# Kernel optimization log

Measured on AMD Instinct MI355X. Metric: run time of the kernel, lower is better.

The kernel has to match this reference:

```python
import jax, jax.numpy as jnp
import numpy as np

B, P, D = 8, 1024, 1024
H, N = 16, 64  # num_heads, head_dim


def setup_inputs() -> dict:
    key = jax.random.key(0)
    k1, k2, k3 = jax.random.split(key, 3)
    inputs = jax.random.normal(k1, (B, P, D), dtype=jnp.float32)
    # Keras 'random_normal' initializer: stddev 0.05
    w_qkv = jax.random.normal(k2, (H, 3, D, N), dtype=jnp.float32) * 0.05
    w_o = jax.random.normal(k3, (N * H, D), dtype=jnp.float32) * 0.05
    return {"inputs": inputs, "w_qkv": w_qkv, "w_o": w_o}


def reference(inputs, w_qkv, w_o):
    # Per-head QKV projection: [b,p,d] x [h,3,d,n] -> [b,h,3,p,n]
    proj = jnp.einsum('bpv,havn->bhapn', inputs, w_qkv)
    q = proj[:, :, 0]  # [b,h,p,n]
    k = proj[:, :, 1]
    v = proj[:, :, 2]
    head_dim = q.shape[-1]
    scale = 1.0 / jnp.sqrt(jnp.asarray(head_dim, dtype=jnp.float32))
    scores = jnp.einsum('bhqn,bhkn->bhqk', q, k) * scale  # [b,h,p,p]
    attn = jax.nn.softmax(scores, axis=-1)
    out = jnp.einsum('bhqk,bhkn->bhqn', attn, v)  # [b,h,p,n]
    # concat heads along feature dim: [b,p,h*n]
    b, h, p, n = out.shape
    concat = out.transpose(0, 2, 1, 3).reshape(b, p, h * n)
    return jnp.einsum('bpi,ij->bpj', concat, w_o)  # [b,p,d_model]
```

## Files before the change

kernel.cpp:

```cpp
#include <hip/hip_runtime.h>
#include <stdint.h>

typedef _Float16 f16;
typedef __attribute__((ext_vector_type(2))) _Float16 f16x2;
typedef __attribute__((ext_vector_type(4))) _Float16 f16x4;
typedef __attribute__((ext_vector_type(8))) _Float16 f16x8;
typedef __attribute__((ext_vector_type(2))) __fp16 h16x2;
typedef __attribute__((ext_vector_type(4))) float f32x4;
typedef __attribute__((ext_vector_type(16))) float f32x16;
typedef __attribute__((ext_vector_type(4))) uint32_t u32x4;

__device__ __forceinline__ void gload_lds16(const void* g, void* l) {
  __builtin_amdgcn_global_load_lds(
      (__attribute__((address_space(1))) void*)const_cast<void*>(g),
      (__attribute__((address_space(3))) void*)l, 16, 0, 0);
}


__global__ void convert_x(const float* __restrict__ in, f16* __restrict__ out) {
  int i = blockIdx.x * 256 + threadIdx.x;
  float4 v = ((const float4*)in)[i];
  f16x4 hv;
  hv[0] = (f16)v.x; hv[1] = (f16)v.y; hv[2] = (f16)v.z; hv[3] = (f16)v.w;
  ((f16x4*)out)[i] = hv;
}

__global__ void transpose_wqkv(const float* __restrict__ in, f16* __restrict__ out) {
  __shared__ float tile[64][65];
  int s = blockIdx.x >> 4;
  int vt = blockIdx.x & 15;
  int hh = s / 3, a = s - hh * 3;
  int tx = threadIdx.x & 63, ty = threadIdx.x >> 6;
#pragma unroll
  for (int i = 0; i < 16; i++) {
    int r = i * 4 + ty;
    tile[r][tx] = in[((size_t)(s * 1024 + vt * 64 + r)) * 64 + tx];
  }
  __syncthreads();
#pragma unroll
  for (int i = 0; i < 16; i++) {
    int n = i * 4 + ty;
    out[((size_t)(a * 1024 + hh * 64 + n)) * 1024 + vt * 64 + tx] = (f16)tile[tx][n];
  }
}

__global__ void transpose_wo(const float* __restrict__ in, f16* __restrict__ out) {
  __shared__ float tile[64][65];
  int rt = blockIdx.x >> 4, ct = blockIdx.x & 15;
  int tx = threadIdx.x & 63, ty = threadIdx.x >> 6;
#pragma unroll
  for (int i = 0; i < 16; i++) {
    int r = i * 4 + ty;
    tile[r][tx] = in[((size_t)(rt * 64 + r)) * 1024 + ct * 64 + tx];
  }
  __syncthreads();
#pragma unroll
  for (int i = 0; i < 16; i++) {
    int j = i * 4 + ty;
    out[((size_t)(ct * 64 + j)) * 1024 + rt * 64 + tx] = (f16)tile[tx][j];
  }
}

template <int OUTMODE>
__global__ __launch_bounds__(256, 4) void gemm_kernel(
    const f16* __restrict__ A, const f16* __restrict__ BT, void* __restrict__ out,
    void* __restrict__ out2, int M, int N, int K) {
  __shared__ __align__(16) f16 As[128][64];
  __shared__ __align__(16) f16 Bs[128][64];
  const int t = threadIdx.x;
  const int lane = t & 63, wave = t >> 6;
  const int lr = lane & 15, lg = lane >> 4;
  const int wm = wave >> 1, wn = wave & 1;
  const int nTN = N >> 7;
  const int bm = blockIdx.x / nTN, bn = blockIdx.x % nTN;
  const f16* Ab = A + (size_t)bm * 128 * K;
  const f16* Bb = BT + (size_t)bn * 128 * K;

  const f32x4 zero4 = {0.f, 0.f, 0.f, 0.f};
  f32x4 acc[4][4];
#pragma unroll
  for (int m = 0; m < 4; m++)
#pragma unroll
    for (int n = 0; n < 4; n++) acc[m][n] = zero4;

  for (int k0 = 0; k0 < K; k0 += 64) {
    __syncthreads();
#pragma unroll
    for (int i = 0; i < 4; i++) {
      int q = wave * 4 + i;
      int u = q * 64 + lane;
      int r = u >> 3, j = u & 7;
      gload_lds16(Ab + (size_t)r * K + k0 + ((j ^ (r & 7)) << 3),
                  (char*)&As[0][0] + q * 1024);
      gload_lds16(Bb + (size_t)r * K + k0 + ((j ^ (r & 7)) << 3),
                  (char*)&Bs[0][0] + q * 1024);
    }
    __syncthreads();
#pragma unroll
    for (int half = 0; half < 2; half++) {
      f16x8 af[4], bf[4];
#pragma unroll
      for (int m = 0; m < 4; m++) {
        int r = wm * 64 + m * 16 + lr;
        af[m] = *(const f16x8*)&As[r][((half * 4 + lg) ^ (r & 7)) << 3];
      }
#pragma unroll
      for (int n = 0; n < 4; n++) {
        int r = wn * 64 + n * 16 + lr;
        bf[n] = *(const f16x8*)&Bs[r][((half * 4 + lg) ^ (r & 7)) << 3];
      }
#pragma unroll
      for (int m = 0; m < 4; m++)
#pragma unroll
        for (int n = 0; n < 4; n++)
          acc[m][n] = __builtin_amdgcn_mfma_f32_16x16x32_f16(af[m], bf[n], acc[m][n], 0, 0, 0);
    }
  }

  const int r0 = bm * 128 + wm * 64;
  const int c0 = bn * 128 + wn * 64;
  if (OUTMODE == 2 && bn >= 16) {
    f16* VT = (f16*)out2;
    const int bb = bm >> 3;
#pragma unroll
    for (int m = 0; m < 4; m++) {
      int pl = (r0 + m * 16 + lg * 4) & 1023;
      int pl2 = (pl & ~12) | ((pl & 4) << 1) | ((pl & 8) >> 1);
#pragma unroll
      for (int n = 0; n < 4; n++) {
        int vcol = c0 - 2048 + n * 16 + lr;
        f16x4 pv;
#pragma unroll
        for (int i = 0; i < 4; i++) pv[i] = (f16)acc[m][n][i];
        *(f16x4*)&VT[((size_t)(bb * 16 + (vcol >> 6)) * 64 + (vcol & 63)) * 1024 + pl2] = pv;
      }
    }
  } else {
#pragma unroll
    for (int m = 0; m < 4; m++)
#pragma unroll
      for (int n = 0; n < 4; n++)
#pragma unroll
        for (int i = 0; i < 4; i++) {
          int gr = r0 + m * 16 + lg * 4 + i;
          int gc = c0 + n * 16 + lr;
          if (OUTMODE == 1)
            ((float*)out)[(size_t)gr * N + gc] = acc[m][n][i];
          else
            ((f16*)out)[(size_t)gr * N + gc] = (f16)acc[m][n][i];
        }
  }
}

__global__ __launch_bounds__(256, 3) void attn_kernel(
    const f16* __restrict__ QKV, const f16* __restrict__ VT, f16* __restrict__ C) {
  __shared__ __align__(16) f16 smem[16384];

  const int t = threadIdx.x, lane = t & 63, wave = t >> 6;
  const int q = lane & 31, hi = lane >> 5, q7 = lane & 7;
  const int pt = blockIdx.x, bh = blockIdx.y;
  const int b = bh >> 4, h = bh & 15;
  const int p0 = pt * 128;

  const f16* Qg = QKV + ((size_t)(b * 1024 + p0)) * 3072 + h * 64;
  const f16* Kg = QKV + ((size_t)(b * 1024)) * 3072 + 1024 + h * 64;
  const f16* Vg = VT + (size_t)bh * 64 * 1024;

#pragma unroll
  for (int i = 0; i < 4; i++) {
    int qn = wave * 4 + i;
    int u = qn * 64 + lane;
    int r = u >> 3, j = u & 7;
    gload_lds16(Qg + (size_t)r * 3072 + ((j ^ (r & 7)) << 3), (char*)smem + qn * 1024);
  }
  __syncthreads();

  const f16 qscale = (f16)0.180336878f;
  f16x8 qB[4];
  {
    int rq = wave * 32 + q;
#pragma unroll
    for (int w = 0; w < 4; w++) {
      int cb = (2 * w + hi) ^ q7;
      f16x8 v = *(const f16x8*)&smem[(size_t)rq * 64 + (cb << 3)];
#pragma unroll
      for (int e = 0; e < 8; e++) v[e] *= qscale;
      qB[w] = v;
    }
  }
  __syncthreads();

  auto STAGE = [&](int kc, int cur) {
#pragma unroll
    for (int i = 0; i < 2; i++) {
      int qn = wave * 2 + i;
      int u = qn * 64 + lane;
      int r = u >> 3, j = u & 7;
      gload_lds16(Kg + (size_t)(kc * 64 + r) * 3072 + ((j ^ (r & 7)) << 3),
                  (char*)smem + cur * 16384 + qn * 1024);
      gload_lds16(Vg + (size_t)r * 1024 + kc * 64 + ((j ^ (r & 7)) << 3),
                  (char*)smem + cur * 16384 + 8192 + qn * 1024);
    }
  };

  STAGE(0, 0);
  STAGE(1, 1);
  asm volatile("s_waitcnt vmcnt(4)" ::: "memory");
  asm volatile("s_barrier" ::: "memory");

  f32x16 o0, o1, ol;
#pragma unroll
  for (int e = 0; e < 16; e++) { o0[e] = 0.f; o1[e] = 0.f; ol[e] = 0.f; }
  float mrun = 0.f;
  const f16x8 ones8 = {(f16)1.f, (f16)1.f, (f16)1.f, (f16)1.f,
                       (f16)1.f, (f16)1.f, (f16)1.f, (f16)1.f};

#pragma unroll 1
  for (int kc = 0; kc < 16; kc++) {
    const int cur = kc & 1;
    const int kB = cur * 8192;
    const int vB = cur * 8192 + 4096;

    f32x16 s0, s1;
#pragma unroll
    for (int e = 0; e < 16; e++) { s0[e] = -mrun; s1[e] = -mrun; }
    __builtin_amdgcn_s_setprio(1);
#pragma unroll
    for (int w = 0; w < 4; w++) {
      int cb = ((2 * w + hi) ^ q7) << 3;
      f16x8 kf0 = *(const f16x8*)&smem[kB + (size_t)q * 64 + cb];
      f16x8 kf1 = *(const f16x8*)&smem[kB + (size_t)(32 + q) * 64 + cb];
      s0 = __builtin_amdgcn_mfma_f32_32x32x16_f16(kf0, qB[w], s0, 0, 0, 0);
      s1 = __builtin_amdgcn_mfma_f32_32x32x16_f16(kf1, qB[w], s1, 0, 0, 0);
    }
    __builtin_amdgcn_s_setprio(0);

    float mx = fmaxf(s0[0], s0[1]);
#pragma unroll
    for (int e = 2; e < 16; e++) mx = fmaxf(mx, s0[e]);
#pragma unroll
    for (int e = 0; e < 16; e++) mx = fmaxf(mx, s1[e]);
    mx = fmaxf(mx, __shfl_xor(mx, 32));
    if (__any(mx > 4.328085f)) {
      float delta = fmaxf(mx, 0.f);
      mrun += delta;
      float alpha = exp2f(-delta);
#pragma unroll
      for (int e = 0; e < 16; e++) {
        s0[e] -= delta; s1[e] -= delta;
        o0[e] *= alpha; o1[e] *= alpha; ol[e] *= alpha;
      }
    }

    f16x8 pb00, pb01, pb10, pb11;
    {
      u32x4 ww;
      ww[0] = __builtin_bit_cast(uint32_t, __builtin_amdgcn_cvt_pkrtz(exp2f(s0[0]), exp2f(s0[1])));
      ww[1] = __builtin_bit_cast(uint32_t, __builtin_amdgcn_cvt_pkrtz(exp2f(s0[2]), exp2f(s0[3])));
      ww[2] = __builtin_bit_cast(uint32_t, __builtin_amdgcn_cvt_pkrtz(exp2f(s0[4]), exp2f(s0[5])));
      ww[3] = __builtin_bit_cast(uint32_t, __builtin_amdgcn_cvt_pkrtz(exp2f(s0[6]), exp2f(s0[7])));
      pb00 = __builtin_bit_cast(f16x8, ww);
      ww[0] = __builtin_bit_cast(uint32_t, __builtin_amdgcn_cvt_pkrtz(exp2f(s0[8]), exp2f(s0[9])));
      ww[1] = __builtin_bit_cast(uint32_t, __builtin_amdgcn_cvt_pkrtz(exp2f(s0[10]), exp2f(s0[11])));
      ww[2] = __builtin_bit_cast(uint32_t, __builtin_amdgcn_cvt_pkrtz(exp2f(s0[12]), exp2f(s0[13])));
      ww[3] = __builtin_bit_cast(uint32_t, __builtin_amdgcn_cvt_pkrtz(exp2f(s0[14]), exp2f(s0[15])));
      pb01 = __builtin_bit_cast(f16x8, ww);
      ww[0] = __builtin_bit_cast(uint32_t, __builtin_amdgcn_cvt_pkrtz(exp2f(s1[0]), exp2f(s1[1])));
      ww[1] = __builtin_bit_cast(uint32_t, __builtin_amdgcn_cvt_pkrtz(exp2f(s1[2]), exp2f(s1[3])));
      ww[2] = __builtin_bit_cast(uint32_t, __builtin_amdgcn_cvt_pkrtz(exp2f(s1[4]), exp2f(s1[5])));
      ww[3] = __builtin_bit_cast(uint32_t, __builtin_amdgcn_cvt_pkrtz(exp2f(s1[6]), exp2f(s1[7])));
      pb10 = __builtin_bit_cast(f16x8, ww);
      ww[0] = __builtin_bit_cast(uint32_t, __builtin_amdgcn_cvt_pkrtz(exp2f(s1[8]), exp2f(s1[9])));
      ww[1] = __builtin_bit_cast(uint32_t, __builtin_amdgcn_cvt_pkrtz(exp2f(s1[10]), exp2f(s1[11])));
      ww[2] = __builtin_bit_cast(uint32_t, __builtin_amdgcn_cvt_pkrtz(exp2f(s1[12]), exp2f(s1[13])));
      ww[3] = __builtin_bit_cast(uint32_t, __builtin_amdgcn_cvt_pkrtz(exp2f(s1[14]), exp2f(s1[15])));
      pb11 = __builtin_bit_cast(f16x8, ww);
    }

    __builtin_amdgcn_s_setprio(1);
    ol = __builtin_amdgcn_mfma_f32_32x32x16_f16(ones8, pb00, ol, 0, 0, 0);
    ol = __builtin_amdgcn_mfma_f32_32x32x16_f16(ones8, pb01, ol, 0, 0, 0);
    ol = __builtin_amdgcn_mfma_f32_32x32x16_f16(ones8, pb10, ol, 0, 0, 0);
    ol = __builtin_amdgcn_mfma_f32_32x32x16_f16(ones8, pb11, ol, 0, 0, 0);
#pragma unroll
    for (int nb = 0; nb < 2; nb++) {
      const int rA = 32 * nb + q;
      f16x8 vf00 = *(const f16x8*)&smem[vB + (size_t)rA * 64 + (((0 + hi) ^ q7) << 3)];
      f16x8 vf01 = *(const f16x8*)&smem[vB + (size_t)rA * 64 + (((2 + hi) ^ q7) << 3)];
      f16x8 vf10 = *(const f16x8*)&smem[vB + (size_t)rA * 64 + (((4 + hi) ^ q7) << 3)];
      f16x8 vf11 = *(const f16x8*)&smem[vB + (size_t)rA * 64 + (((6 + hi) ^ q7) << 3)];
      if (nb == 0) {
        o0 = __builtin_amdgcn_mfma_f32_32x32x16_f16(vf00, pb00, o0, 0, 0, 0);
        o0 = __builtin_amdgcn_mfma_f32_32x32x16_f16(vf01, pb01, o0, 0, 0, 0);
        o0 = __builtin_amdgcn_mfma_f32_32x32x16_f16(vf10, pb10, o0, 0, 0, 0);
        o0 = __builtin_amdgcn_mfma_f32_32x32x16_f16(vf11, pb11, o0, 0, 0, 0);
      } else {
        o1 = __builtin_amdgcn_mfma_f32_32x32x16_f16(vf00, pb00, o1, 0, 0, 0);
        o1 = __builtin_amdgcn_mfma_f32_32x32x16_f16(vf01, pb01, o1, 0, 0, 0);
        o1 = __builtin_amdgcn_mfma_f32_32x32x16_f16(vf10, pb10, o1, 0, 0, 0);
        o1 = __builtin_amdgcn_mfma_f32_32x32x16_f16(vf11, pb11, o1, 0, 0, 0);
      }
    }
    __builtin_amdgcn_s_setprio(0);

    asm volatile("s_waitcnt lgkmcnt(0)\n\ts_barrier" ::: "memory");
    if (kc + 2 < 16) {
      STAGE(kc + 2, cur);
      asm volatile("s_waitcnt vmcnt(4)" ::: "memory");
    } else {
      asm volatile("s_waitcnt vmcnt(0)" ::: "memory");
    }
    asm volatile("s_barrier" ::: "memory");
  }

  {
    float li = 1.f / ol[0];
    const int row = wave * 32 + q;
    const int px = q7 << 3;
#pragma unroll
    for (int rp = 0; rp < 8; rp++) {
      int r = 2 * rp;
      int n0 = (r & 3) + 8 * (r >> 2) + 4 * hi;
      uint32_t w0 = __builtin_bit_cast(uint32_t,
          __builtin_amdgcn_cvt_pkrtz(o0[r] * li, o0[r + 1] * li));
      uint32_t w1 = __builtin_bit_cast(uint32_t,
          __builtin_amdgcn_cvt_pkrtz(o1[r] * li, o1[r + 1] * li));
      *(uint32_t*)&smem[(size_t)row * 64 + (n0 ^ px)] = w0;
      *(uint32_t*)&smem[(size_t)row * 64 + ((n0 + 32) ^ px)] = w1;
    }
  }
  __syncthreads();
  {
    const int c = t & 7;
#pragma unroll
    for (int i = 0; i < 4; i++) {
      int row = (t >> 3) + 32 * i;
      f16x8 rd = *(const f16x8*)&smem[(size_t)row * 64 + ((c ^ (row & 7)) << 3)];
      *(f16x8*)&C[((size_t)(b * 1024 + p0 + row)) * 1024 + h * 64 + c * 8] = rd;
    }
  }
}

extern "C" void kernel_launch(void* const* d_in, const int* in_sizes, int n_in,
                              void* d_out, int out_size, void* d_ws, size_t ws_size,
                              hipStream_t stream) {
  const float* X = (const float*)d_in[0];
  const float* Wqkv = (const float*)d_in[1];
  const float* Wo = (const float*)d_in[2];
  float* Y = (float*)d_out;

  f16* ws = (f16*)d_ws;
  f16* X16 = ws;
  f16* WqkvT = ws + 8388608;
  f16* WoT = ws + 11534336;
  f16* QKV = ws + 12582912;
  f16* VT = (f16*)d_out;

  convert_x<<<8192, 256, 0, stream>>>(X, X16);
  transpose_wqkv<<<768, 256, 0, stream>>>(Wqkv, WqkvT);
  transpose_wo<<<256, 256, 0, stream>>>(Wo, WoT);
  gemm_kernel<2><<<64 * 24, 256, 0, stream>>>(X16, WqkvT, QKV, VT, 8192, 3072, 1024);
  attn_kernel<<<dim3(8, 128), 256, 0, stream>>>(QKV, VT, X16 );
  gemm_kernel<1><<<64 * 8, 256, 0, stream>>>(X16 , WoT, Y, nullptr, 8192, 1024, 1024);
}
```

Measured before the change: 177.1 us.

## Add 256x256-tile QKV GEMM kernel and change attention LDS swizzle

Replaces the 128x128-tile QKV projection GEMM with a new 512-thread kernel using 256x256 tiles. It double-buffers K slices in LDS, interleaves prefetch with MFMA work, and remaps workgroups across the 8 XCDs. The aim is more operand reuse per LDS load and fewer global loads. The attention kernel's LDS XOR swizzle now also mixes in bits 3-5 of the row, to cut bank conflicts between rows 32 apart. In exchange the new GEMM uses 128KB of LDS and more registers per workgroup, and launches only 384 workgroups, which may underfill the GPU.

```diff
diff --git a/kernel.cpp b/kernel.cpp
--- a/kernel.cpp
+++ b/kernel.cpp
@@ -2,10 +2,8 @@
 #include <stdint.h>
 
 typedef _Float16 f16;
-typedef __attribute__((ext_vector_type(2))) _Float16 f16x2;
 typedef __attribute__((ext_vector_type(4))) _Float16 f16x4;
 typedef __attribute__((ext_vector_type(8))) _Float16 f16x8;
-typedef __attribute__((ext_vector_type(2))) __fp16 h16x2;
 typedef __attribute__((ext_vector_type(4))) float f32x4;
 typedef __attribute__((ext_vector_type(16))) float f32x16;
 typedef __attribute__((ext_vector_type(4))) uint32_t u32x4;
@@ -119,16 +117,121 @@
 
   const int r0 = bm * 128 + wm * 64;
   const int c0 = bn * 128 + wn * 64;
-  if (OUTMODE == 2 && bn >= 16) {
+#pragma unroll
+  for (int m = 0; m < 4; m++)
+#pragma unroll
+    for (int n = 0; n < 4; n++)
+#pragma unroll
+      for (int i = 0; i < 4; i++) {
+        int gr = r0 + m * 16 + lg * 4 + i;
+        int gc = c0 + n * 16 + lr;
+        if (OUTMODE == 1)
+          ((float*)out)[(size_t)gr * N + gc] = acc[m][n][i];
+        else
+          ((f16*)out)[(size_t)gr * N + gc] = (f16)acc[m][n][i];
+      }
+}
+
+template <int OUTMODE>
+__global__ __launch_bounds__(512, 2) void gemm256_kernel(
+    const f16* __restrict__ A, const f16* __restrict__ BT, void* __restrict__ out,
+    void* __restrict__ out2, int M, int N, int K) {
+  __shared__ __align__(16) f16 smem[65536];
+  const int t = threadIdx.x;
+  const int lane = t & 63, wave = t >> 6;
+  const int lr = lane & 15, lg = lane >> 4;
+  const int wm = wave >> 2, wn = wave & 3;
+  const int nTN = N >> 8;
+  const int nwg = gridDim.x;
+  const int cpx = nwg >> 3;
+  const int wg = (blockIdx.x & 7) * cpx + (blockIdx.x >> 3);
+  const int bm = wg / nTN, bn = wg % nTN;
+  const f16* Ab = A + (size_t)bm * 256 * K;
+  const f16* Bb = BT + (size_t)bn * 256 * K;
+
+  auto STAGE = [&](const f16* srcb, int chunk, int dstF16) {
+    int u = chunk * 512 + t;
+    int r = u >> 3, j = u & 7;
+    gload_lds16(srcb + (size_t)r * K + ((j ^ (r & 7)) << 3),
+                (char*)smem + (size_t)dstF16 * 2 + (size_t)chunk * 8192 + wave * 1024);
+  };
+
+  const f32x4 zero4 = {0.f, 0.f, 0.f, 0.f};
+  f32x4 acc[8][4];
+#pragma unroll
+  for (int m = 0; m < 8; m++)
+#pragma unroll
+    for (int n = 0; n < 4; n++) acc[m][n] = zero4;
+
+#pragma unroll
+  for (int c = 0; c < 4; c++) {
+    STAGE(Ab, c, 0);
+    STAGE(Bb, c, 32768);
+  }
+  asm volatile("s_waitcnt vmcnt(0)" ::: "memory");
+  __builtin_amdgcn_s_barrier();
+
+  const int NT = K >> 6;
+#pragma unroll 1
+  for (int kt = 0; kt < NT; kt++) {
+    const int cur = kt & 1;
+    const int aB = cur * 16384, bB = 32768 + cur * 16384;
+    const int aN = (cur ^ 1) * 16384, bN = 32768 + (cur ^ 1) * 16384;
+    const f16* An = Ab + (kt + 1) * 64;
+    const f16* Bn = Bb + (kt + 1) * 64;
+    const bool pf = (kt + 1) < NT;
+
+    f16x8 bf[4][2];
+#pragma unroll
+    for (int q = 0; q < 4; q++) {
+      if (pf) {
+        STAGE(An, q, aN);
+        STAGE(Bn, q, bN);
+      }
+      if (q == 0) {
+#pragma unroll
+        for (int n = 0; n < 4; n++)
+#pragma unroll
+          for (int ks = 0; ks < 2; ks++) {
+            int R = wn * 64 + n * 16 + lr;
+            bf[n][ks] = *(const f16x8*)&smem[bB + (size_t)R * 64 + (((ks * 4 + lg) ^ (R & 7)) << 3)];
+          }
+      }
+      f16x8 af[2][2];
+#pragma unroll
+      for (int mi = 0; mi < 2; mi++)
+#pragma unroll
+        for (int ks = 0; ks < 2; ks++) {
+          int R = wm * 128 + (q * 2 + mi) * 16 + lr;
+          af[mi][ks] = *(const f16x8*)&smem[aB + (size_t)R * 64 + (((ks * 4 + lg) ^ (R & 7)) << 3)];
+        }
+      __builtin_amdgcn_s_setprio(1);
+#pragma unroll
+      for (int mi = 0; mi < 2; mi++)
+#pragma unroll
+        for (int n = 0; n < 4; n++)
+#pragma unroll
+          for (int ks = 0; ks < 2; ks++)
+            acc[q * 2 + mi][n] = __builtin_amdgcn_mfma_f32_16x16x32_f16(
+                af[mi][ks], bf[n][ks], acc[q * 2 + mi][n], 0, 0, 0);
+      __builtin_amdgcn_s_setprio(0);
+    }
+    asm volatile("s_waitcnt vmcnt(0)" ::: "memory");
+    __builtin_amdgcn_s_barrier();
+  }
+
+  const int r0 = bm * 256 + wm * 128;
+  const int c0 = bn * 256 + wn * 64;
+  if (OUTMODE == 2 && bn >= 8) {
     f16* VT = (f16*)out2;
-    const int bb = bm >> 3;
-#pragma unroll
-    for (int m = 0; m < 4; m++) {
+    const int bb = bm >> 2;
+#pragma unroll
+    for (int m = 0; m < 8; m++) {
       int pl = (r0 + m * 16 + lg * 4) & 1023;
       int pl2 = (pl & ~12) | ((pl & 4) << 1) | ((pl & 8) >> 1);
 #pragma unroll
       for (int n = 0; n < 4; n++) {
-        int vcol = c0 - 2048 + n * 16 + lr;
+        int vcol = (bn - 8) * 256 + wn * 64 + n * 16 + lr;
         f16x4 pv;
 #pragma unroll
         for (int i = 0; i < 4; i++) pv[i] = (f16)acc[m][n][i];
@@ -137,7 +240,7 @@
     }
   } else {
 #pragma unroll
-    for (int m = 0; m < 4; m++)
+    for (int m = 0; m < 8; m++)
 #pragma unroll
       for (int n = 0; n < 4; n++)
 #pragma unroll
@@ -157,7 +260,7 @@
   __shared__ __align__(16) f16 smem[16384];
 
   const int t = threadIdx.x, lane = t & 63, wave = t >> 6;
-  const int q = lane & 31, hi = lane >> 5, q7 = lane & 7;
+  const int q = lane & 31, hi = lane >> 5;
   const int pt = blockIdx.x, bh = blockIdx.y;
   const int b = bh >> 4, h = bh & 15;
   const int p0 = pt * 128;
@@ -171,7 +274,8 @@
     int qn = wave * 4 + i;
     int u = qn * 64 + lane;
     int r = u >> 3, j = u & 7;
-    gload_lds16(Qg + (size_t)r * 3072 + ((j ^ (r & 7)) << 3), (char*)smem + qn * 1024);
+    int fr = (r ^ (r >> 3)) & 7;
+    gload_lds16(Qg + (size_t)r * 3072 + ((j ^ fr) << 3), (char*)smem + qn * 1024);
   }
   __syncthreads();
 
@@ -179,9 +283,10 @@
   f16x8 qB[4];
   {
     int rq = wave * 32 + q;
+    int fq = (rq ^ (rq >> 3)) & 7;
 #pragma unroll
     for (int w = 0; w < 4; w++) {
-      int cb = (2 * w + hi) ^ q7;
+      int cb = (2 * w + hi) ^ fq;
       f16x8 v = *(const f16x8*)&smem[(size_t)rq * 64 + (cb << 3)];
 #pragma unroll
       for (int e = 0; e < 8; e++) v[e] *= qscale;
@@ -196,9 +301,10 @@
       int qn = wave * 2 + i;
       int u = qn * 64 + lane;
       int r = u >> 3, j = u & 7;
-      gload_lds16(Kg + (size_t)(kc * 64 + r) * 3072 + ((j ^ (r & 7)) << 3),
+      int fr = (r ^ (r >> 3)) & 7;
+      gload_lds16(Kg + (size_t)(kc * 64 + r) * 3072 + ((j ^ fr) << 3),
                   (char*)smem + cur * 16384 + qn * 1024);
-      gload_lds16(Vg + (size_t)r * 1024 + kc * 64 + ((j ^ (r & 7)) << 3),
+      gload_lds16(Vg + (size_t)r * 1024 + kc * 64 + ((j ^ fr) << 3),
                   (char*)smem + cur * 16384 + 8192 + qn * 1024);
     }
   };
@@ -214,6 +320,8 @@
   float mrun = 0.f;
   const f16x8 ones8 = {(f16)1.f, (f16)1.f, (f16)1.f, (f16)1.f,
                        (f16)1.f, (f16)1.f, (f16)1.f, (f16)1.f};
+  const int fk0 = (q ^ (q >> 3)) & 7;
+  const int fk1 = fk0 ^ 4;
 
 #pragma unroll 1
   for (int kc = 0; kc < 16; kc++) {
@@ -227,9 +335,9 @@
     __builtin_amdgcn_s_setprio(1);
 #pragma unroll
     for (int w = 0; w < 4; w++) {
-      int cb = ((2 * w + hi) ^ q7) << 3;
-      f16x8 kf0 = *(const f16x8*)&smem[kB + (size_t)q * 64 + cb];
-      f16x8 kf1 = *(const f16x8*)&smem[kB + (size_t)(32 + q) * 64 + cb];
+      int cb = 2 * w + hi;
+      f16x8 kf0 = *(const f16x8*)&smem[kB + (size_t)q * 64 + ((cb ^ fk0) << 3)];
+      f16x8 kf1 = *(const f16x8*)&smem[kB + (size_t)(32 + q) * 64 + ((cb ^ fk1) << 3)];
       s0 = __builtin_amdgcn_mfma_f32_32x32x16_f16(kf0, qB[w], s0, 0, 0, 0);
       s1 = __builtin_amdgcn_mfma_f32_32x32x16_f16(kf1, qB[w], s1, 0, 0, 0);
     }
@@ -285,10 +393,11 @@
 #pragma unroll
     for (int nb = 0; nb < 2; nb++) {
       const int rA = 32 * nb + q;
-      f16x8 vf00 = *(const f16x8*)&smem[vB + (size_t)rA * 64 + (((0 + hi) ^ q7) << 3)];
-      f16x8 vf01 = *(const f16x8*)&smem[vB + (size_t)rA * 64 + (((2 + hi) ^ q7) << 3)];
-      f16x8 vf10 = *(const f16x8*)&smem[vB + (size_t)rA * 64 + (((4 + hi) ^ q7) << 3)];
-      f16x8 vf11 = *(const f16x8*)&smem[vB + (size_t)rA * 64 + (((6 + hi) ^ q7) << 3)];
+      const int fv = nb ? fk1 : fk0;
+      f16x8 vf00 = *(const f16x8*)&smem[vB + (size_t)rA * 64 + (((0 + hi) ^ fv) << 3)];
+      f16x8 vf01 = *(const f16x8*)&smem[vB + (size_t)rA * 64 + (((2 + hi) ^ fv) << 3)];
+      f16x8 vf10 = *(const f16x8*)&smem[vB + (size_t)rA * 64 + (((4 + hi) ^ fv) << 3)];
+      f16x8 vf11 = *(const f16x8*)&smem[vB + (size_t)rA * 64 + (((6 + hi) ^ fv) << 3)];
       if (nb == 0) {
         o0 = __builtin_amdgcn_mfma_f32_32x32x16_f16(vf00, pb00, o0, 0, 0, 0);
         o0 = __builtin_amdgcn_mfma_f32_32x32x16_f16(vf01, pb01, o0, 0, 0, 0);
@@ -316,7 +425,7 @@
   {
     float li = 1.f / ol[0];
     const int row = wave * 32 + q;
-    const int px = q7 << 3;
+    const int px = (q & 7) << 3;
 #pragma unroll
     for (int rp = 0; rp < 8; rp++) {
       int r = 2 * rp;
@@ -359,7 +468,7 @@
   convert_x<<<8192, 256, 0, stream>>>(X, X16);
   transpose_wqkv<<<768, 256, 0, stream>>>(Wqkv, WqkvT);
   transpose_wo<<<256, 256, 0, stream>>>(Wo, WoT);
-  gemm_kernel<2><<<64 * 24, 256, 0, stream>>>(X16, WqkvT, QKV, VT, 8192, 3072, 1024);
+  gemm256_kernel<2><<<384, 512, 0, stream>>>(X16, WqkvT, QKV, VT, 8192, 3072, 1024);
   attn_kernel<<<dim3(8, 128), 256, 0, stream>>>(QKV, VT, X16 );
   gemm_kernel<1><<<64 * 8, 256, 0, stream>>>(X16 , WoT, Y, nullptr, 8192, 1024, 1024);
 }
```

After: 183.0 us. 3.3% more time.
